# Performance work log

Measured on AMD Instinct MI355X. Metric: run time of the kernel, lower is better.

## Reference

```python
import jax, jax.numpy as jnp
import numpy as np

HEADS = 16


def bemm(x, weight, bias, er, es):
    # BatchEnsembleMM.forward: x [T,B,Hin], weight [Hout,Hin], er [B,Hin], es [B,Hout]
    x_r = x * er[None, :, :]
    x_mm = jnp.einsum('tbh,oh->tbo', x_r, weight)
    return x_mm * es[None, :, :] + bias


def rel_shift(x):
    # RelativeShift.forward (batch_first): x [N, len_q, len_r]
    n, q, r = x.shape
    x_pad = jnp.pad(x, ((0, 0), (0, 0), (1, 0)))        # [N, q, r+1]
    x_view = x_pad.reshape(n, r + 1, q)[:, 1:, :]        # drop first 'row'
    return x_view.reshape(n, q, r)


def setup_inputs() -> dict:
    key = jax.random.key(0)
    ks = jax.random.split(key, 14)
    T, B, H = 1024, 8, 1024
    Lr = 1024
    s = 0.02
    return {
        'inputs': jax.random.normal(ks[0], (T, B, H), jnp.float32),
        'pos': jax.random.normal(ks[1], (Lr, 1, H), jnp.float32),
        'input_weights': jax.random.normal(ks[2], (3 * H, H), jnp.float32) * s,
        'input_biases': jax.random.normal(ks[3], (3 * H,), jnp.float32) * s,
        'pos_weights': jax.random.normal(ks[4], (H, H), jnp.float32) * s,
        'pos_biases': jax.random.normal(ks[5], (H,), jnp.float32) * s,
        'output_weights': jax.random.normal(ks[6], (H, H), jnp.float32) * s,
        'output_biases': jax.random.normal(ks[7], (H,), jnp.float32) * s,
        'r_i': 1.0 + jax.random.normal(ks[8], (B, H), jnp.float32) * 0.1,
        's_i': 1.0 + jax.random.normal(ks[9], (B, 3 * H), jnp.float32) * 0.1,
        'r_p': 1.0 + jax.random.normal(ks[10], (B, H), jnp.float32) * 0.1,
        's_p': 1.0 + jax.random.normal(ks[11], (B, H), jnp.float32) * 0.1,
        'r_w_bias': jax.random.normal(ks[12], (HEADS, H // HEADS), jnp.float32) * s,
        'r_r_bias': jax.random.normal(ks[13], (HEADS, H // HEADS), jnp.float32) * s,
        'heads': HEADS,
    }


def reference(inputs, pos, input_weights, input_biases, pos_weights, pos_biases,
              output_weights, output_biases, r_i, s_i, r_p, s_p,
              r_w_bias, r_r_bias, heads):
    T, B, H = inputs.shape
    hd = H // heads
    scale = hd ** (-0.5)
    Lr = pos.shape[0]

    pos_rep = jnp.broadcast_to(pos, (Lr, B, H))

    # BatchEnsemble QKV and positional projections (training path)
    qkv = bemm(inputs, input_weights, input_biases, r_i, s_i)       # [T,B,3H]
    qkv = qkv.reshape(T, B * heads, 3, hd)
    queries, keys, values = qkv[:, :, 0, :], qkv[:, :, 1, :], qkv[:, :, 2, :]

    r_head_k = bemm(pos_rep, pos_weights, pos_biases, r_p, s_p)     # [Lr,B,H]
    r_head_k = r_head_k.reshape(Lr, B * heads, hd)

    rw_head_q = (queries.reshape(T, B, heads, hd) + r_w_bias).reshape(T, B * heads, hd)
    rr_head_q = (queries.reshape(T, B, heads, hd) + r_r_bias).reshape(T, B * heads, hd)

    # content score AC and position score BD
    matmul_ac = jnp.einsum('qnd,knd->nqk', rw_head_q, keys) * scale    # [B*h,T,T]
    matmul_bd = jnp.einsum('qnd,rnd->nqr', rr_head_q, r_head_k) * scale
    matmul_bd = rel_shift(matmul_bd)[:, :, :T]

    attn_score = matmul_ac + matmul_bd
    softmax_results = jax.nn.softmax(attn_score.astype(jnp.float32), axis=-1).astype(inputs.dtype)

    context = jnp.einsum('nqk,knd->qnd', softmax_results, values).reshape(T, B, H)
    outputs = jnp.einsum('tbh,oh->tbo', context, output_weights) + output_biases
    return outputs
```

## Files before the change

### kernel.cpp

```cpp
#include <hip/hip_runtime.h>
#include <cstdint>
#include <cstddef>

using u16 = unsigned short;
typedef short short8 __attribute__((ext_vector_type(8)));
typedef short short4v __attribute__((ext_vector_type(4)));
typedef unsigned short us8 __attribute__((ext_vector_type(8)));
typedef unsigned short us4 __attribute__((ext_vector_type(4)));
typedef float f32x4 __attribute__((ext_vector_type(4)));
typedef float f4 __attribute__((ext_vector_type(4)));

#define T_ 1024
#define B_ 8
#define H_ 1024
#define HEADS_ 16
#define HD_ 64
#define N3_ 3072

__device__ __forceinline__ float b2f(u16 u){
  union { float f; unsigned int i; } v; v.i = ((unsigned int)u) << 16; return v.f;
}
__device__ __forceinline__ u16 f2b(float f){
  union { float f; unsigned int i; } v; v.f = f;
  return (u16)((v.i + 0x8000u) >> 16);
}

template<bool HAS_S, bool SCALE_A, bool POS_A, bool A_BF16, bool OUT_F32>
__global__ __launch_bounds__(256) void k_gemm(const void* __restrict__ A_, const float* __restrict__ W,
                                              const float* __restrict__ RA, const float* __restrict__ S,
                                              const float* __restrict__ bias, void* __restrict__ C_, int N){
  const int K = 1024;
  const int n0 = blockIdx.x * 128, m0 = blockIdx.y * 128;
  const int tid = threadIdx.x, lane = tid & 63;
  const int wave = tid >> 6, wr = wave >> 1, wc = wave & 1;
  __shared__ alignas(16) u16 At[128 * 32];
  __shared__ alignas(16) u16 Bt[128 * 32];
  f32x4 acc[4][4] = {};

  for (int kt = 0; kt < 32; ++kt){
    const int k0 = kt * 32;
    f4 wv[4];
    us8 avb[2];
    f4 avf[4];
#pragma unroll
    for (int i = 0; i < 4; ++i){
      int c = tid + i * 256, r = c >> 3, sg = c & 7;
      wv[i] = *(const f4*)(W + (size_t)(n0 + r) * K + k0 + sg * 4);
    }
    if (A_BF16){
      const u16* A = (const u16*)A_;
#pragma unroll
      for (int i = 0; i < 2; ++i){
        int c = tid + i * 256, r = c >> 2, sg = c & 3;
        avb[i] = *(const us8*)(A + (size_t)(m0 + r) * K + k0 + sg * 8);
      }
    } else {
      const float* A = (const float*)A_;
#pragma unroll
      for (int i = 0; i < 4; ++i){
        int c = tid + i * 256, r = c >> 3, sg = c & 7;
        int m = m0 + r;
        const float* ap = POS_A ? (A + (size_t)(m >> 3) * K + k0 + sg * 4)
                                : (A + (size_t)m * K + k0 + sg * 4);
        avf[i] = *(const f4*)ap;
        if (SCALE_A){
          f4 rv = *(const f4*)(RA + (m & 7) * K + k0 + sg * 4);
          avf[i] = avf[i] * rv;
        }
      }
    }
    __syncthreads();
#pragma unroll
    for (int i = 0; i < 4; ++i){
      int c = tid + i * 256, r = c >> 3, sg = c & 7;
      us4 pw;
#pragma unroll
      for (int u = 0; u < 4; ++u) pw[u] = f2b(wv[i][u]);
      *(us4*)(Bt + r * 32 + sg * 4) = pw;
    }
    if (A_BF16){
#pragma unroll
      for (int i = 0; i < 2; ++i){
        int c = tid + i * 256, r = c >> 2, sg = c & 3;
        *(us8*)(At + r * 32 + sg * 8) = avb[i];
      }
    } else {
#pragma unroll
      for (int i = 0; i < 4; ++i){
        int c = tid + i * 256, r = c >> 3, sg = c & 7;
        us4 pa;
#pragma unroll
        for (int u = 0; u < 4; ++u) pa[u] = f2b(avf[i][u]);
        *(us4*)(At + r * 32 + sg * 4) = pa;
      }
    }
    __syncthreads();
    short8 af[4], bf[4];
#pragma unroll
    for (int i = 0; i < 4; ++i){
      int ar = wr * 64 + i * 16 + (lane & 15);
      af[i] = *(const short8*)(At + ar * 32 + ((lane >> 4) << 3));
      int br = wc * 64 + i * 16 + (lane & 15);
      bf[i] = *(const short8*)(Bt + br * 32 + ((lane >> 4) << 3));
    }
#pragma unroll
    for (int i = 0; i < 4; ++i)
#pragma unroll
      for (int j = 0; j < 4; ++j)
        acc[i][j] = __builtin_amdgcn_mfma_f32_16x16x32_bf16(af[i], bf[j], acc[i][j], 0, 0, 0);
  }
#pragma unroll
  for (int i = 0; i < 4; ++i){
    int row0 = wr * 64 + i * 16 + ((lane >> 4) << 2);
#pragma unroll
    for (int j = 0; j < 4; ++j){
      int o = n0 + wc * 64 + j * 16 + (lane & 15);
      float bv = bias[o];
#pragma unroll
      for (int jj = 0; jj < 4; ++jj){
        int m = m0 + row0 + jj;
        float v = acc[i][j][jj];
        if (HAS_S) v *= S[(m & 7) * N + o];
        v += bv;
        if (OUT_F32) ((float*)C_)[(size_t)m * N + o] = v;
        else         ((u16*)C_)[(size_t)m * N + o] = f2b(v);
      }
    }
  }
}

__global__ __launch_bounds__(256) void k_vt(const u16* __restrict__ qkv, u16* __restrict__ VT){
  const int tt = blockIdx.x;
  const int n = blockIdx.y;
  const int b = n >> 4, head = n & 15;
  __shared__ alignas(16) u16 tile[64][72];
  const int tid = threadIdx.x;
#pragma unroll
  for (int i = 0; i < 2; ++i){
    int c = tid + i * 256;
    int r = c >> 3, sg = c & 7;
    const u16* src = qkv + ((size_t)(tt * 64 + r) * 8 + b) * N3_ + head * 192 + 128 + sg * 8;
    *(us8*)&tile[r][sg * 8] = *(const us8*)src;
  }
  __syncthreads();
#pragma unroll
  for (int i = 0; i < 2; ++i){
    int c = tid + i * 256;
    int d = c >> 3, sg = c & 7;
    us8 ov;
#pragma unroll
    for (int u = 0; u < 8; ++u) ov[u] = tile[sg * 8 + u][d];
    *(us8*)(VT + ((size_t)n * 64 + d) * 1024 + tt * 64 + sg * 8) = ov;
  }
}

#define G_OFF   0
#define RWQ_OFF 67664
#define RRQ_OFF 71760
#define RED_OFF 77904
#define SMEM_SZ 79952

__device__ __forceinline__ int gswz(int byt){
  return byt ^ (((byt >> 11) & 1) << 2) ^ (((byt >> 13) & 3) << 5);
}

__global__ __launch_bounds__(512) __attribute__((amdgpu_waves_per_eu(4)))
void k_attn(const u16* __restrict__ qkv, const u16* __restrict__ rk,
            const u16* __restrict__ VTg, const float* __restrict__ rwb,
            const float* __restrict__ rrb, u16* __restrict__ ctx){
  const int bid = blockIdx.x;
  const int n = (bid & 7) + ((bid >> 8) << 3);
  const int qb = (bid >> 3) & 31;
  const int q0 = qb * 32;
  const int bat = n >> 4, head = n & 15;
  const int tid = threadIdx.x, lane = tid & 63, wave = tid >> 6;
  const int l15 = lane & 15, grp = lane >> 4;

  __shared__ alignas(16) char smem[SMEM_SZ];
  char* gB  = smem + G_OFF;
  u16* rwq = (u16*)(smem + RWQ_OFF);
  u16* rrq = (u16*)(smem + RRQ_OFF);
  float* redf = (float*)(smem + RED_OFF);

  const float PRESCALE = 0.125f * 1.44269504089f;
#pragma unroll
  for (int rep = 0; rep < 2; ++rep){
    int c = tid + rep * 512;
    if (c < 640){
      int s = c >> 3, sg = c & 7;
      u16* dst; int row; const float* bias;
      if (s < 32){ dst = rwq; row = s; bias = rwb; }
      else       { dst = rrq; row = s - 32; bias = rrb; }
      int qrow = q0 + row;
      float v[8];
      const float* bp2 = bias + head * 64 + sg * 8;
      if (qrow < T_){
        const u16* qp = qkv + ((size_t)qrow * 8 + bat) * N3_ + head * 192 + sg * 8;
        us8 qv = *(const us8*)qp;
        f4 b0 = *(const f4*)bp2, b1 = *(const f4*)(bp2 + 4);
#pragma unroll
        for (int u = 0; u < 4; ++u){
          v[u]     = (b2f(qv[u])     + b0[u]) * PRESCALE;
          v[u + 4] = (b2f(qv[u + 4]) + b1[u]) * PRESCALE;
        }
      } else {
#pragma unroll
        for (int u = 0; u < 8; ++u) v[u] = 0.f;
      }
      us8 pk;
#pragma unroll
      for (int u = 0; u < 8; ++u) pk[u] = f2b(v[u]);
      *(us8*)((char*)dst + row * 128 + ((sg * 16) ^ ((row & 7) << 4))) = pk;
    }
  }
  if (tid < 33) *(u16*)(gB + gswz(tid * 2050 + 2048)) = 0;

  auto ldf = [&](const void* base, int row, int kkb)->short8 {
    int co = kkb + (grp << 4);
    return *(const short8*)((const char*)base + row * 128 + (co ^ ((row & 7) << 4)));
  };

  __syncthreads();

  {
    short8 af[3][2];
#pragma unroll
    for (int pi = 0; pi < 3; ++pi)
#pragma unroll
      for (int kk = 0; kk < 2; ++kk) af[pi][kk] = ldf(rrq, pi * 16 + l15, kk * 64);
#pragma unroll
    for (int s = 0; s < 2; ++s){
#pragma unroll
      for (int c4 = 0; c4 < 4; ++c4){
        int r = s * 512 + wave * 64 + c4 * 16 + l15;
        const u16* bp = rk + ((size_t)r * 8 + bat) * 1024 + head * 64 + grp * 8;
        short8 bf0 = *(const short8*)bp;
        short8 bf1 = *(const short8*)(bp + 32);
#pragma unroll
        for (int pi = 0; pi < 3; ++pi){
          f32x4 acc = {0.f, 0.f, 0.f, 0.f};
          acc = __builtin_amdgcn_mfma_f32_16x16x32_bf16(af[pi][0], bf0, acc, 0, 0, 0);
          acc = __builtin_amdgcn_mfma_f32_16x16x32_bf16(af[pi][1], bf1, acc, 0, 0, 0);
#pragma unroll
          for (int jj = 0; jj < 4; ++jj){
            int a = pi * 16 + (grp << 2) + jj;
            if (a < 33) *(u16*)(gB + gswz(a * 2050 + (r << 1))) = f2b(acc[jj]);
          }
        }
      }
    }
  }
  __syncthreads();

  short8 qf[2][2];
#pragma unroll
  for (int m = 0; m < 2; ++m)
#pragma unroll
    for (int kk = 0; kk < 2; ++kk) qf[m][kk] = ldf(rwq, m * 16 + l15, kk * 64);

  float m_run[2] = {-3.0e38f, -3.0e38f};
  float l_run[2] = {0.f, 0.f};
  f32x4 Oacc[2][4] = {};

#pragma unroll
  for (int pr = 0; pr < 4; ++pr){
    int base = wave * 64 + (pr & 1) * 32 + (pr >> 1) * 512;
    float s_[2][2][4];
#pragma unroll
    for (int h = 0; h < 2; ++h){
      int cb = base + h * 16;
      const u16* kp = qkv + ((size_t)(cb + l15) * 8 + bat) * N3_ + head * 192 + 64 + grp * 8;
      short8 kf0 = *(const short8*)kp;
      short8 kf1 = *(const short8*)(kp + 32);
#pragma unroll
      for (int m = 0; m < 2; ++m){
        f32x4 acc = {0.f, 0.f, 0.f, 0.f};
        acc = __builtin_amdgcn_mfma_f32_16x16x32_bf16(kf0, qf[m][0], acc, 0, 0, 0);
        acc = __builtin_amdgcn_mfma_f32_16x16x32_bf16(kf1, qf[m][1], acc, 0, 0, 0);
        int aa = m * 16 + l15;
#pragma unroll
        for (int jj = 0; jj < 4; ++jj){
          int bcol = cb + (grp << 2) + jj;
          int byt = (aa << 11) + ((1023 - q0 + bcol) << 1);
          s_[h][m][jj] = acc[jj] + b2f(*(const u16*)(gB + gswz(byt)));
        }
      }
    }
    float cm[2];
#pragma unroll
    for (int m = 0; m < 2; ++m){
      float c0 = fmaxf(fmaxf(s_[0][m][0], s_[0][m][1]), fmaxf(s_[0][m][2], s_[0][m][3]));
      float c1 = fmaxf(fmaxf(s_[1][m][0], s_[1][m][1]), fmaxf(s_[1][m][2], s_[1][m][3]));
      float c = fmaxf(c0, c1);
      c = fmaxf(c, __shfl_xor(c, 16));
      c = fmaxf(c, __shfl_xor(c, 32));
      cm[m] = c;
    }
    if (!__all(cm[0] <= m_run[0] + 8.f && cm[1] <= m_run[1] + 8.f)){
#pragma unroll
      for (int m = 0; m < 2; ++m){
        float mn = fmaxf(m_run[m], cm[m]);
        float f = __builtin_exp2f(m_run[m] - mn);
        l_run[m] *= f;
        m_run[m] = mn;
#pragma unroll
        for (int jj = 0; jj < 4; ++jj){
          float fq = __shfl(f, (lane & 48) + ((lane >> 2) & 12) + jj);
#pragma unroll
          for (int dt = 0; dt < 4; ++dt) Oacc[m][dt][jj] *= fq;
        }
      }
    }
    short8 pa[2];
#pragma unroll
    for (int m = 0; m < 2; ++m){
      float ls = 0.f;
#pragma unroll
      for (int jj = 0; jj < 4; ++jj){
        float e0 = __builtin_exp2f(s_[0][m][jj] - m_run[m]);
        float e1 = __builtin_exp2f(s_[1][m][jj] - m_run[m]);
        ls += e0 + e1;
        pa[m][jj]     = (short)f2b(e0);
        pa[m][4 + jj] = (short)f2b(e1);
      }
      l_run[m] += ls;
    }
#pragma unroll
    for (int dt = 0; dt < 4; ++dt){
      const u16* vp = VTg + ((size_t)n * 64 + dt * 16 + l15) * 1024 + base + (grp << 2);
      short4v v0 = *(const short4v*)vp;
      short4v v1 = *(const short4v*)(vp + 16);
      short8 vb = {v0[0], v0[1], v0[2], v0[3], v1[0], v1[1], v1[2], v1[3]};
#pragma unroll
      for (int m = 0; m < 2; ++m)
        Oacc[m][dt] = __builtin_amdgcn_mfma_f32_16x16x32_bf16(pa[m], vb, Oacc[m][dt], 0, 0, 0);
    }
  }

#pragma unroll
  for (int m = 0; m < 2; ++m){
    l_run[m] += __shfl_xor(l_run[m], 16);
    l_run[m] += __shfl_xor(l_run[m], 32);
  }
  if (grp == 0){
#pragma unroll
    for (int m = 0; m < 2; ++m){
      redf[wave * 32 + m * 16 + l15] = m_run[m];
      redf[256 + wave * 32 + m * 16 + l15] = l_run[m];
    }
  }
  __syncthreads();

  float* par = (float*)(smem + wave * 8192);
#pragma unroll
  for (int m = 0; m < 2; ++m)
#pragma unroll
    for (int dt = 0; dt < 4; ++dt)
#pragma unroll
      for (int jj = 0; jj < 4; ++jj)
        par[(m * 16 + (grp << 2) + jj) * 64 + dt * 16 + l15] = Oacc[m][dt][jj];
  __syncthreads();

  {
    float* parAll = (float*)smem;
    int q = tid >> 4, d4 = (tid & 15) * 4;
    float M = -3.0e38f;
#pragma unroll
    for (int w = 0; w < 8; ++w) M = fmaxf(M, redf[w * 32 + q]);
    f32x4 v = {0.f, 0.f, 0.f, 0.f};
    float L = 0.f;
#pragma unroll
    for (int w = 0; w < 8; ++w){
      float sc = __builtin_exp2f(redf[w * 32 + q] - M);
      L += redf[256 + w * 32 + q] * sc;
      f32x4 pv = *(const f32x4*)(parAll + w * 2048 + q * 64 + d4);
      v += pv * sc;
    }
    float il = 1.0f / (L + 1e-20f);
    us4 pk;
#pragma unroll
    for (int e = 0; e < 4; ++e) pk[e] = f2b(v[e] * il);
    *(us4*)(ctx + ((size_t)(q0 + q) * 8 + bat) * 1024 + head * 64 + d4) = pk;
  }
}

extern "C" void kernel_launch(void* const* d_in, const int* in_sizes, int n_in,
                              void* d_out, int out_size, void* d_ws, size_t ws_size,
                              hipStream_t stream){
  const float* x   = (const float*)d_in[0];
  const float* pos = (const float*)d_in[1];
  const float* Wi  = (const float*)d_in[2];
  const float* bi  = (const float*)d_in[3];
  const float* Wp  = (const float*)d_in[4];
  const float* bp  = (const float*)d_in[5];
  const float* Wo  = (const float*)d_in[6];
  const float* bo  = (const float*)d_in[7];
  const float* r_i = (const float*)d_in[8];
  const float* s_i = (const float*)d_in[9];
  const float* r_p = (const float*)d_in[10];
  const float* s_p = (const float*)d_in[11];
  const float* rwb = (const float*)d_in[12];
  const float* rrb = (const float*)d_in[13];

  const size_t MB = 1024 * 1024;
  u16* qkv = (u16*)((char*)d_ws);
  u16* rk  = (u16*)((char*)d_ws + 48 * MB);
  u16* VTg  = (u16*)d_out;
  u16* ctxg = (u16*)((char*)d_out + 16777216);

  k_gemm<true,  true,  false, false, false><<<dim3(24, 64), 256, 0, stream>>>(x,   Wi, r_i, s_i, bi, qkv, N3_);
  k_gemm<true,  true,  true,  false, false><<<dim3(8, 64),  256, 0, stream>>>(pos, Wp, r_p, s_p, bp, rk, 1024);
  k_vt<<<dim3(16, 128), 256, 0, stream>>>(qkv, VTg);
  k_attn<<<dim3(4096), 512, 0, stream>>>(qkv, rk, VTg, rwb, rrb, ctxg);
  hipMemcpyAsync(qkv, ctxg, (size_t)out_size * sizeof(u16), hipMemcpyDeviceToDevice, stream);
  k_gemm<false, false, false, true, true><<<dim3(8, 64), 256, 0, stream>>>(qkv, Wo, nullptr, nullptr, bo, (float*)d_out, 1024);
}
```

Baseline: 452.3 us.

## Prescale input to bf16, use global_load_lds for bf16 A, drop LDS swizzle

Adds a pre-pass kernel that multiplies the input by r_i and stores it as bf16, so the QKV GEMM reads half-width A and can use global_load_lds to copy A straight into shared memory, skipping the register round trip. In the attention kernel it removes the XOR swizzle on the positional-score LDS buffer and precomputes base offsets. It also changes how the V fragment is assembled. The trade-offs are an extra kernel launch and pass over the input, and possible LDS bank conflicts once the swizzle is gone.

```diff
diff --git a/kernel.cpp b/kernel.cpp
--- a/kernel.cpp
+++ b/kernel.cpp
@@ -23,6 +23,25 @@
 __device__ __forceinline__ u16 f2b(float f){
   union { float f; unsigned int i; } v; v.f = f;
   return (u16)((v.i + 0x8000u) >> 16);
+}
+typedef __attribute__((address_space(1))) const void gvoid;
+typedef __attribute__((address_space(3))) void lvoid;
+__device__ __forceinline__ void gload16(const void* g, void* l){
+  __builtin_amdgcn_global_load_lds((gvoid*)g, (lvoid*)l, 16, 0, 0);
+}
+
+__global__ __launch_bounds__(256) void k_scaleA(const float* __restrict__ x, const float* __restrict__ r,
+                                                u16* __restrict__ o){
+  int idx = blockIdx.x * 256 + threadIdx.x;
+  int base = idx * 8;
+  int h = base & (H_ - 1);
+  int b = (base >> 10) & (B_ - 1);
+  f4 x0 = *(const f4*)(x + base), x1 = *(const f4*)(x + base + 4);
+  f4 r0 = *(const f4*)(r + b * H_ + h), r1 = *(const f4*)(r + b * H_ + h + 4);
+  us8 ov;
+#pragma unroll
+  for (int u = 0; u < 4; ++u){ ov[u] = f2b(x0[u] * r0[u]); ov[u + 4] = f2b(x1[u] * r1[u]); }
+  *(us8*)(o + base) = ov;
 }
 
 template<bool HAS_S, bool SCALE_A, bool POS_A, bool A_BF16, bool OUT_F32>
@@ -40,21 +59,13 @@
   for (int kt = 0; kt < 32; ++kt){
     const int k0 = kt * 32;
     f4 wv[4];
-    us8 avb[2];
     f4 avf[4];
 #pragma unroll
     for (int i = 0; i < 4; ++i){
       int c = tid + i * 256, r = c >> 3, sg = c & 7;
       wv[i] = *(const f4*)(W + (size_t)(n0 + r) * K + k0 + sg * 4);
     }
-    if (A_BF16){
-      const u16* A = (const u16*)A_;
-#pragma unroll
-      for (int i = 0; i < 2; ++i){
-        int c = tid + i * 256, r = c >> 2, sg = c & 3;
-        avb[i] = *(const us8*)(A + (size_t)(m0 + r) * K + k0 + sg * 8);
-      }
-    } else {
+    if (!A_BF16){
       const float* A = (const float*)A_;
 #pragma unroll
       for (int i = 0; i < 4; ++i){
@@ -70,6 +81,14 @@
       }
     }
     __syncthreads();
+    if (A_BF16){
+      const u16* A = (const u16*)A_;
+#pragma unroll
+      for (int i = 0; i < 2; ++i){
+        int c = tid + i * 256, r = c >> 2, sg = c & 3;
+        gload16(A + (size_t)(m0 + r) * K + k0 + sg * 8, (char*)At + (size_t)c * 16);
+      }
+    }
 #pragma unroll
     for (int i = 0; i < 4; ++i){
       int c = tid + i * 256, r = c >> 3, sg = c & 7;
@@ -78,13 +97,7 @@
       for (int u = 0; u < 4; ++u) pw[u] = f2b(wv[i][u]);
       *(us4*)(Bt + r * 32 + sg * 4) = pw;
     }
-    if (A_BF16){
-#pragma unroll
-      for (int i = 0; i < 2; ++i){
-        int c = tid + i * 256, r = c >> 2, sg = c & 3;
-        *(us8*)(At + r * 32 + sg * 8) = avb[i];
-      }
-    } else {
+    if (!A_BF16){
 #pragma unroll
       for (int i = 0; i < 4; ++i){
         int c = tid + i * 256, r = c >> 3, sg = c & 7;
@@ -159,10 +172,6 @@
 #define RRQ_OFF 71760
 #define RED_OFF 77904
 #define SMEM_SZ 79952
-
-__device__ __forceinline__ int gswz(int byt){
-  return byt ^ (((byt >> 11) & 1) << 2) ^ (((byt >> 13) & 3) << 5);
-}
 
 __global__ __launch_bounds__(512) __attribute__((amdgpu_waves_per_eu(4)))
 void k_attn(const u16* __restrict__ qkv, const u16* __restrict__ rk,
@@ -213,7 +222,7 @@
       *(us8*)((char*)dst + row * 128 + ((sg * 16) ^ ((row & 7) << 4))) = pk;
     }
   }
-  if (tid < 33) *(u16*)(gB + gswz(tid * 2050 + 2048)) = 0;
+  if (tid < 33) *(u16*)(gB + tid * 2050 + 2048) = 0;
 
   auto ldf = [&](const void* base, int row, int kkb)->short8 {
     int co = kkb + (grp << 4);
@@ -228,6 +237,7 @@
     for (int pi = 0; pi < 3; ++pi)
 #pragma unroll
       for (int kk = 0; kk < 2; ++kk) af[pi][kk] = ldf(rrq, pi * 16 + l15, kk * 64);
+    const int sbase = (grp * 4) * 2050 + ((wave * 64 + l15) << 1);
 #pragma unroll
     for (int s = 0; s < 2; ++s){
 #pragma unroll
@@ -244,7 +254,8 @@
 #pragma unroll
           for (int jj = 0; jj < 4; ++jj){
             int a = pi * 16 + (grp << 2) + jj;
-            if (a < 33) *(u16*)(gB + gswz(a * 2050 + (r << 1))) = f2b(acc[jj]);
+            if (a < 33)
+              *(u16*)(gB + sbase + (pi * 16 + jj) * 2050 + ((s * 512 + c4 * 16) << 1)) = f2b(acc[jj]);
           }
         }
       }
@@ -261,6 +272,8 @@
   float m_run[2] = {-3.0e38f, -3.0e38f};
   float l_run[2] = {0.f, 0.f};
   f32x4 Oacc[2][4] = {};
+
+  const int gthr = (l15 << 11) + ((1023 - q0 + wave * 64 + (grp << 2)) << 1);
 
 #pragma unroll
   for (int pr = 0; pr < 4; ++pr){
@@ -277,12 +290,10 @@
         f32x4 acc = {0.f, 0.f, 0.f, 0.f};
         acc = __builtin_amdgcn_mfma_f32_16x16x32_bf16(kf0, qf[m][0], acc, 0, 0, 0);
         acc = __builtin_amdgcn_mfma_f32_16x16x32_bf16(kf1, qf[m][1], acc, 0, 0, 0);
-        int aa = m * 16 + l15;
 #pragma unroll
         for (int jj = 0; jj < 4; ++jj){
-          int bcol = cb + (grp << 2) + jj;
-          int byt = (aa << 11) + ((1023 - q0 + bcol) << 1);
-          s_[h][m][jj] = acc[jj] + b2f(*(const u16*)(gB + gswz(byt)));
+          int off = (m << 15) + (((pr & 1) * 32 + (pr >> 1) * 512 + h * 16 + jj) << 1);
+          s_[h][m][jj] = acc[jj] + b2f(*(const u16*)(gB + gthr + off));
         }
       }
     }
@@ -328,9 +339,9 @@
 #pragma unroll
     for (int dt = 0; dt < 4; ++dt){
       const u16* vp = VTg + ((size_t)n * 64 + dt * 16 + l15) * 1024 + base + (grp << 2);
-      short4v v0 = *(const short4v*)vp;
-      short4v v1 = *(const short4v*)(vp + 16);
-      short8 vb = {v0[0], v0[1], v0[2], v0[3], v1[0], v1[1], v1[2], v1[3]};
+      short8 vb;
+      *(short4v*)&vb = *(const short4v*)vp;
+      *((short4v*)&vb + 1) = *(const short4v*)(vp + 16);
 #pragma unroll
       for (int m = 0; m < 2; ++m)
         Oacc[m][dt] = __builtin_amdgcn_mfma_f32_16x16x32_bf16(pa[m], vb, Oacc[m][dt], 0, 0, 0);
@@ -405,13 +416,15 @@
   const size_t MB = 1024 * 1024;
   u16* qkv = (u16*)((char*)d_ws);
   u16* rk  = (u16*)((char*)d_ws + 48 * MB);
+  u16* Ai   = (u16*)d_out;
   u16* VTg  = (u16*)d_out;
   u16* ctxg = (u16*)((char*)d_out + 16777216);
 
-  k_gemm<true,  true,  false, false, false><<<dim3(24, 64), 256, 0, stream>>>(x,   Wi, r_i, s_i, bi, qkv, N3_);
-  k_gemm<true,  true,  true,  false, false><<<dim3(8, 64),  256, 0, stream>>>(pos, Wp, r_p, s_p, bp, rk, 1024);
+  k_scaleA<<<dim3(4096), 256, 0, stream>>>(x, r_i, Ai);
+  k_gemm<true,  false, false, true,  false><<<dim3(24, 64), 256, 0, stream>>>(Ai,  Wi, nullptr, s_i, bi, qkv, N3_);
+  k_gemm<true,  true,  true,  false, false><<<dim3(8, 64),  256, 0, stream>>>(pos, Wp, r_p,    s_p, bp, rk, 1024);
   k_vt<<<dim3(16, 128), 256, 0, stream>>>(qkv, VTg);
   k_attn<<<dim3(4096), 512, 0, stream>>>(qkv, rk, VTg, rwb, rrb, ctxg);
   hipMemcpyAsync(qkv, ctxg, (size_t)out_size * sizeof(u16), hipMemcpyDeviceToDevice, stream);
-  k_gemm<false, false, false, true, true><<<dim3(8, 64), 256, 0, stream>>>(qkv, Wo, nullptr, nullptr, bo, (float*)d_out, 1024);
-}
+  k_gemm<false, false, false, true,  true ><<<dim3(8, 64),  256, 0, stream>>>(qkv, Wo, nullptr, nullptr, bo, (float*)d_out, 1024);
+}
```

Result: no change. 446.9 us (-1.2%).
